# Optimization experiments

Measured on AMD Instinct MI355X. Metric: run time of the kernel, lower is better.

Reference implementation:

```python
import jax, jax.numpy as jnp
import numpy as np

B, N, IN, H, DK, DV, OUT = 8, 1024, 512, 8, 64, 64, 512
SCALE = 1.0 / (DK ** 0.5)


def setup_inputs() -> dict:
    key = jax.random.key(0)
    ks = jax.random.split(key, 10)
    s = lambda fan_in: 1.0 / np.sqrt(fan_in)
    return {
        "x": jax.random.normal(ks[0], (B, N, IN), dtype=jnp.float32),
        "Wv": jax.random.uniform(ks[1], (IN, H * DV), jnp.float32, -s(IN), s(IN)),
        "bv": jax.random.uniform(ks[2], (H * DV,), jnp.float32, -s(IN), s(IN)),
        "Wk": jax.random.uniform(ks[3], (IN, H * DK), jnp.float32, -s(IN), s(IN)),
        "bk": jax.random.uniform(ks[4], (H * DK,), jnp.float32, -s(IN), s(IN)),
        "Wq": jax.random.uniform(ks[5], (IN, H * DK), jnp.float32, -s(IN), s(IN)),
        "bq": jax.random.uniform(ks[6], (H * DK,), jnp.float32, -s(IN), s(IN)),
        "Wo": jax.random.uniform(ks[7], (H * DV, OUT), jnp.float32, -s(H * DV), s(H * DV)),
        "bo": jax.random.uniform(ks[8], (OUT,), jnp.float32, -s(H * DV), s(H * DV)),
        "mask": jax.random.randint(ks[9], (B, N, N), 0, 2, dtype=jnp.int32),
    }


def reference(x, Wv, bv, Wk, bk, Wq, bq, Wo, bo, mask):
    # projections -> (B, N, H, d), vkq activation = relu
    v = jax.nn.relu((x @ Wv + bv).reshape(B, N, H, DV))
    q = jax.nn.relu((x @ Wq + bq).reshape(B, N, H, DK))
    k = jax.nn.relu((x @ Wk + bk).reshape(B, N, H, DK))
    # (B, H, N, d)
    q, k, v = (t.transpose(0, 2, 1, 3) for t in (q, k, v))
    # raw attention weights (returned pre-mask, pre-softmax): (B, H, N, N)
    att_weights = jnp.einsum("bhqd,bhkd->bhqk", q, k) * SCALE
    att = jnp.where(mask[:, None, :, :] == 0, -1e9, att_weights)
    att = jax.nn.softmax(att, axis=-1)
    out = jnp.einsum("bhqk,bhkd->bhqd", att, v) + v  # residual add of v
    out = out.transpose(0, 2, 1, 3).reshape(B, N, H * DV)
    out = jax.nn.relu(out @ Wo + bo)  # final activation = relu
    return out, att_weights
```

## Files before the change

kernel.cpp:

```cpp
#include <hip/hip_runtime.h>
#include <hip/hip_bf16.h>

typedef __attribute__((ext_vector_type(8))) short short8;
typedef __attribute__((ext_vector_type(4))) float f32x4;

#define DEV static __device__ __forceinline__

DEV unsigned short f2bf(float f) {
  union { float f; unsigned u; } v; v.f = f;
  unsigned r = v.u + 0x7FFFu + ((v.u >> 16) & 1u);
  return (unsigned short)(r >> 16);
}
DEV float bf2f(unsigned short b) {
  union { unsigned u; float f; } v; v.u = ((unsigned)b) << 16;
  return v.f;
}

DEV unsigned cvtpk_bf16(float lo, float hi) {
  unsigned r;
  asm("v_cvt_pk_bf16_f32 %0, %1, %2" : "=v"(r) : "v"(lo), "v"(hi));
  return r;
}

DEV void gld_lds16(const void* g, void* l) {
  __builtin_amdgcn_global_load_lds(
      (const __attribute__((address_space(1))) unsigned int*)g,
      (__attribute__((address_space(3))) unsigned int*)l, 16, 0, 0);
}

DEV short8 lds_read8(const unsigned short* base, int byteoff) {
  return *reinterpret_cast<const short8*>(reinterpret_cast<const char*>(base) + byteoff);
}

__global__ __launch_bounds__(256) void cast_x_kernel(const float* __restrict__ x,
                                                     unsigned short* __restrict__ xb, int n4) {
  int i = blockIdx.x * blockDim.x + threadIdx.x;
  if (i >= n4) return;
  float4 v = reinterpret_cast<const float4*>(x)[i];
  ushort4 o;
  o.x = f2bf(v.x); o.y = f2bf(v.y); o.z = f2bf(v.z); o.w = f2bf(v.w);
  reinterpret_cast<ushort4*>(xb)[i] = o;
}

__global__ __launch_bounds__(256) void mask_prep_kernel(const int* __restrict__ mask,
                                                        unsigned char* __restrict__ mb) {
  int i = blockIdx.x * 256 + threadIdx.x;
  int4 m4 = reinterpret_cast<const int4*>(mask)[i];
  unsigned v = (m4.x ? 1u : 0u) | ((m4.y ? 1u : 0u) << 8) |
               ((m4.z ? 1u : 0u) << 16) | ((m4.w ? 1u : 0u) << 24);
  reinterpret_cast<unsigned*>(mb)[i] = v;
}

__global__ __launch_bounds__(256) void transpose_w_kernel(
    const float* __restrict__ W0, const float* __restrict__ W1,
    const float* __restrict__ W2, const float* __restrict__ W3,
    unsigned short* __restrict__ T0, unsigned short* __restrict__ T1,
    unsigned short* __restrict__ T2, unsigned short* __restrict__ T3) {
  const float* W = blockIdx.z == 0 ? W0 : blockIdx.z == 1 ? W1 : blockIdx.z == 2 ? W2 : W3;
  unsigned short* T = blockIdx.z == 0 ? T0 : blockIdx.z == 1 ? T1 : blockIdx.z == 2 ? T2 : T3;
  __shared__ unsigned short tile[32][33];
  int tx = threadIdx.x & 31, ty = threadIdx.x >> 5;
  int n0 = blockIdx.x * 32, k0 = blockIdx.y * 32;
#pragma unroll
  for (int i = 0; i < 32; i += 8)
    tile[ty + i][tx] = f2bf(W[(size_t)(k0 + ty + i) * 512 + n0 + tx]);
  __syncthreads();
#pragma unroll
  for (int i = 0; i < 32; i += 8)
    T[(size_t)(n0 + ty + i) * 512 + k0 + tx] = tile[tx][ty + i];
}

__global__ __launch_bounds__(256) void gemm_proj_kernel(
    const unsigned short* __restrict__ xb,
    const unsigned short* __restrict__ WqT, const unsigned short* __restrict__ WkT,
    const unsigned short* __restrict__ WvT,
    const float* __restrict__ bq, const float* __restrict__ bk, const float* __restrict__ bv,
    unsigned short* __restrict__ qn, unsigned short* __restrict__ kn,
    unsigned short* __restrict__ vn, unsigned short* __restrict__ vT) {
  const int z = blockIdx.z;
  const unsigned short* Wt = z == 0 ? WqT : z == 1 ? WkT : WvT;
  const float* bias = z == 0 ? bq : z == 1 ? bk : bv;
  unsigned short* outp = z == 0 ? qn : z == 1 ? kn : vn;

  __shared__ unsigned short smem[17408];
  unsigned short* As = smem;
  unsigned short* Bs = smem + 4096;

  const int tid = threadIdx.x;
  const int lane = tid & 63;
  const int w = tid >> 6;
  const int wm = w >> 1, wn = w & 1;
  const int lr = lane & 15;
  const int g = lane >> 4;

  const int m0 = blockIdx.x * 128;
  const int n0 = blockIdx.y * 128;

  f32x4 acc[4][4];
#pragma unroll
  for (int i = 0; i < 4; ++i)
#pragma unroll
    for (int j = 0; j < 4; ++j) acc[i][j] = (f32x4){0.f, 0.f, 0.f, 0.f};

  for (int kt = 0; kt < 16; ++kt) {
    const int k0 = kt * 32;
    __syncthreads();
#pragma unroll
    for (int p = 0; p < 2; ++p) {
      int slot = tid + 256 * p;
      int r = slot >> 2;
      int kg = (slot & 3) ^ ((r >> 1) & 3);
      unsigned short* ldsA = As + (size_t)((tid >> 6) + 4 * p) * 512;
      unsigned short* ldsB = Bs + (size_t)((tid >> 6) + 4 * p) * 512;
      gld_lds16(xb + (size_t)(m0 + r) * 512 + k0 + kg * 8, ldsA);
      gld_lds16(Wt + (size_t)(n0 + r) * 512 + k0 + kg * 8, ldsB);
    }
    __syncthreads();
    short8 af[4], bfr[4];
#pragma unroll
    for (int mi = 0; mi < 4; ++mi) {
      int r = wm * 64 + mi * 16 + lr;
      af[mi] = lds_read8(As, (r * 64 + g * 16) ^ (((r >> 1) & 3) << 4));
    }
#pragma unroll
    for (int ni = 0; ni < 4; ++ni) {
      int r = wn * 64 + ni * 16 + lr;
      bfr[ni] = lds_read8(Bs, (r * 64 + g * 16) ^ (((r >> 1) & 3) << 4));
    }
#pragma unroll
    for (int mi = 0; mi < 4; ++mi)
#pragma unroll
      for (int ni = 0; ni < 4; ++ni)
        acc[mi][ni] = __builtin_amdgcn_mfma_f32_16x16x32_bf16(af[mi], bfr[ni], acc[mi][ni], 0, 0, 0);
  }
  __syncthreads();

  float biasv[4];
#pragma unroll
  for (int ni = 0; ni < 4; ++ni) biasv[ni] = bias[n0 + wn * 64 + ni * 16 + lr];

#pragma unroll
  for (int mi = 0; mi < 4; ++mi) {
    int rowb = m0 + wm * 64 + mi * 16 + g * 4;
#pragma unroll
    for (int ni = 0; ni < 4; ++ni) {
      int c = n0 + wn * 64 + ni * 16 + lr;
      int h = c >> 6, d = c & 63;
#pragma unroll
      for (int rr = 0; rr < 4; ++rr) {
        float vf = acc[mi][ni][rr] + biasv[ni];
        vf = vf > 0.f ? vf : 0.f;
        unsigned short bvv = f2bf(vf);
        int row = rowb + rr;
        int b = row >> 10, tok = row & 1023;
        outp[((size_t)(b * 8 + h) * 1024 + tok) * 64 + d] = bvv;
        if (z == 2) {
          int cl = wn * 64 + ni * 16 + lr;
          int rl = wm * 64 + mi * 16 + g * 4 + rr;
          smem[cl * 136 + rl] = bvv;
        }
      }
    }
  }
  if (z == 2) {
    __syncthreads();
    int cl = tid >> 1, half = tid & 1;
    int gc = n0 + cl, h = gc >> 6, d = gc & 63;
    int b = m0 >> 10;
    int tokbase = (m0 & 1023) + half * 64;
    size_t base = (size_t)(b * 8 + h) * 65536 + (size_t)d * 1024 + tokbase;
    const unsigned short* src = smem + cl * 136 + half * 64;
#pragma unroll
    for (int j = 0; j < 8; ++j) {
      short8 v8 = *reinterpret_cast<const short8*>(src + j * 8);
      *reinterpret_cast<short8*>(vT + base + j * 8) = v8;
    }
  }
}

__global__ __launch_bounds__(256) void attn_kernel(
    const unsigned short* __restrict__ qg, const unsigned short* __restrict__ kgp,
    const unsigned short* __restrict__ vg, const unsigned short* __restrict__ vTg,
    const unsigned char* __restrict__ mb, float* __restrict__ attw,
    unsigned short* __restrict__ Og) {
  __shared__ unsigned short Ks[2][4096];
  __shared__ unsigned short Vs[2][4096];
  __shared__ unsigned short Ps[4096];

  const int tid = threadIdx.x, lane = tid & 63, w = tid >> 6;
  const int lr = lane & 15, g = lane >> 4;

  const int bid = blockIdx.x;
  const int b = bid & 7;
  const int idx = bid >> 3;
  const int h = idx >> 4;
  const int qc = idx & 15;
  const int bh = b * 8 + h;

  const int qw = qc * 64 + w * 16;
  const size_t qbase = (size_t)bh * 65536;
  const int gq = qw + lr;

  const unsigned short* kbase = kgp + qbase;
  const unsigned short* vbase = vTg + qbase;

  const int srow0 = w * 8 + (lane >> 3);
  const int sseg = lane & 7;

  short8 aq[2];
#pragma unroll
  for (int dc = 0; dc < 2; ++dc)
    aq[dc] = *reinterpret_cast<const short8*>(qg + qbase + (size_t)gq * 64 + dc * 32 + g * 8);

  f32x4 o[4];
#pragma unroll
  for (int di = 0; di < 4; ++di) o[di] = (f32x4){0.f, 0.f, 0.f, 0.f};
  float lsum = 0.f;

  unsigned short* Pw = Ps + w * 1024;
  const unsigned char* mp = mb + ((size_t)(b * 1024 + gq)) * 1024 + g * 4;
  float* awp = attw + ((size_t)bh * 1024 + gq) * 1024 + g * 4;

#pragma unroll
  for (int p = 0; p < 2; ++p) {
    int rr = srow0 + 32 * p;
    int sk = sseg ^ (rr & 7);
    gld_lds16(kbase + (size_t)rr * 64 + sk * 8, reinterpret_cast<char*>(Ks[0]) + (w + 4 * p) * 1024);
    gld_lds16(vbase + (size_t)rr * 1024 + sk * 8, reinterpret_cast<char*>(Vs[0]) + (w + 4 * p) * 1024);
  }
  asm volatile("s_waitcnt vmcnt(0)" ::: "memory");
  __builtin_amdgcn_sched_barrier(0);
  __builtin_amdgcn_s_barrier();

  int cur = 0;
  for (int t = 0; t < 16; ++t) {
    const int kv0 = t * 64;

    unsigned mk[4];
#pragma unroll
    for (int ni = 0; ni < 4; ++ni)
      mk[ni] = *reinterpret_cast<const unsigned*>(mp + kv0 + ni * 16);
    __builtin_amdgcn_sched_barrier(0);

    if (t < 15) {
      const int kn0 = kv0 + 64;
      unsigned short* Kn = Ks[cur ^ 1];
      unsigned short* Vn = Vs[cur ^ 1];
#pragma unroll
      for (int p = 0; p < 2; ++p) {
        int rr = srow0 + 32 * p;
        int sk = sseg ^ (rr & 7);
        gld_lds16(kbase + (size_t)(kn0 + rr) * 64 + sk * 8,
                  reinterpret_cast<char*>(Kn) + (w + 4 * p) * 1024);
        gld_lds16(vbase + (size_t)rr * 1024 + kn0 + sk * 8,
                  reinterpret_cast<char*>(Vn) + (w + 4 * p) * 1024);
      }
    }
    __builtin_amdgcn_sched_barrier(0);

    const unsigned short* Kc = Ks[cur];
    const unsigned short* Vc = Vs[cur];

    f32x4 s[4];
    __builtin_amdgcn_s_setprio(1);
#pragma unroll
    for (int ni = 0; ni < 4; ++ni) {
      int row = ni * 16 + lr;
      s[ni] = (f32x4){0.f, 0.f, 0.f, 0.f};
#pragma unroll
      for (int dc = 0; dc < 2; ++dc) {
        short8 ak = lds_read8(Kc, (row * 128 + dc * 64 + g * 16) ^ ((row & 7) << 4));
        s[ni] = __builtin_amdgcn_mfma_f32_16x16x32_bf16(ak, aq[dc], s[ni], 0, 0, 0);
      }
    }
    __builtin_amdgcn_s_setprio(0);

#pragma unroll
    for (int ni = 0; ni < 4; ++ni) {
      f32x4 sv = s[ni] * 0.125f;
      *reinterpret_cast<f32x4*>(awp + kv0 + ni * 16) = sv;
      unsigned m = mk[ni];
      float p0 = (m & 0x000000FFu) ? __expf(sv[0] - 16.f) : 0.f;
      float p1 = (m & 0x0000FF00u) ? __expf(sv[1] - 16.f) : 0.f;
      float p2 = (m & 0x00FF0000u) ? __expf(sv[2] - 16.f) : 0.f;
      float p3 = (m & 0xFF000000u) ? __expf(sv[3] - 16.f) : 0.f;
      lsum += (p0 + p1) + (p2 + p3);
      uint2 pk = make_uint2(cvtpk_bf16(p0, p1), cvtpk_bf16(p2, p3));
      int pbyte = (lr * 128 + ni * 32 + g * 8) ^ ((lr & 7) << 4);
      *reinterpret_cast<uint2*>(reinterpret_cast<char*>(Pw) + pbyte) = pk;
    }

    __builtin_amdgcn_s_setprio(1);
#pragma unroll
    for (int kc = 0; kc < 2; ++kc) {
      short8 ap = lds_read8(Pw, (lr * 128 + kc * 64 + g * 16) ^ ((lr & 7) << 4));
#pragma unroll
      for (int di = 0; di < 4; ++di) {
        int rd = di * 16 + lr;
        short8 bv8 = lds_read8(Vc, (rd * 128 + kc * 64 + g * 16) ^ ((rd & 7) << 4));
        o[di] = __builtin_amdgcn_mfma_f32_16x16x32_bf16(ap, bv8, o[di], 0, 0, 0);
      }
    }
    __builtin_amdgcn_s_setprio(0);

    asm volatile("s_waitcnt vmcnt(4)" ::: "memory");
    __builtin_amdgcn_sched_barrier(0);
    __builtin_amdgcn_s_barrier();
    __builtin_amdgcn_sched_barrier(0);
    cur ^= 1;
  }

  float l = lsum;
  l += __shfl_xor(l, 16);
  l += __shfl_xor(l, 32);

#pragma unroll
  for (int rr = 0; rr < 4; ++rr) {
    int gq2 = qw + g * 4 + rr;
    float lq = __shfl(l, g * 4 + rr);
    float inv = 1.f / lq;
#pragma unroll
    for (int di = 0; di < 4; ++di) {
      int gd = di * 16 + lr;
      float ov = o[di][rr] * inv + bf2f(vg[qbase + (size_t)gq2 * 64 + gd]);
      Og[((size_t)(b * 1024 + gq2)) * 512 + h * 64 + gd] = f2bf(ov);
    }
  }
}

__global__ __launch_bounds__(256) void gemm_out_kernel(
    const unsigned short* __restrict__ Ab, const unsigned short* __restrict__ WoT,
    const float* __restrict__ bo, float* __restrict__ outp) {
  __shared__ unsigned short smem[8192];
  unsigned short* As = smem;
  unsigned short* Bs = smem + 4096;

  const int tid = threadIdx.x;
  const int lane = tid & 63;
  const int w = tid >> 6;
  const int wm = w >> 1, wn = w & 1;
  const int lr = lane & 15;
  const int g = lane >> 4;
  const int m0 = blockIdx.x * 128;
  const int n0 = blockIdx.y * 128;

  f32x4 acc[4][4];
#pragma unroll
  for (int i = 0; i < 4; ++i)
#pragma unroll
    for (int j = 0; j < 4; ++j) acc[i][j] = (f32x4){0.f, 0.f, 0.f, 0.f};

  for (int kt = 0; kt < 16; ++kt) {
    const int k0 = kt * 32;
    __syncthreads();
#pragma unroll
    for (int p = 0; p < 2; ++p) {
      int slot = tid + 256 * p;
      int r = slot >> 2;
      int kg = (slot & 3) ^ ((r >> 1) & 3);
      unsigned short* ldsA = As + (size_t)((tid >> 6) + 4 * p) * 512;
      unsigned short* ldsB = Bs + (size_t)((tid >> 6) + 4 * p) * 512;
      gld_lds16(Ab + (size_t)(m0 + r) * 512 + k0 + kg * 8, ldsA);
      gld_lds16(WoT + (size_t)(n0 + r) * 512 + k0 + kg * 8, ldsB);
    }
    __syncthreads();
    short8 af[4], bfr[4];
#pragma unroll
    for (int mi = 0; mi < 4; ++mi) {
      int r = wm * 64 + mi * 16 + lr;
      af[mi] = lds_read8(As, (r * 64 + g * 16) ^ (((r >> 1) & 3) << 4));
    }
#pragma unroll
    for (int ni = 0; ni < 4; ++ni) {
      int r = wn * 64 + ni * 16 + lr;
      bfr[ni] = lds_read8(Bs, (r * 64 + g * 16) ^ (((r >> 1) & 3) << 4));
    }
#pragma unroll
    for (int mi = 0; mi < 4; ++mi)
#pragma unroll
      for (int ni = 0; ni < 4; ++ni)
        acc[mi][ni] = __builtin_amdgcn_mfma_f32_16x16x32_bf16(af[mi], bfr[ni], acc[mi][ni], 0, 0, 0);
  }

  float biasv[4];
#pragma unroll
  for (int ni = 0; ni < 4; ++ni) biasv[ni] = bo[n0 + wn * 64 + ni * 16 + lr];
#pragma unroll
  for (int mi = 0; mi < 4; ++mi) {
    int rowb = m0 + wm * 64 + mi * 16 + g * 4;
#pragma unroll
    for (int ni = 0; ni < 4; ++ni) {
      int c = n0 + wn * 64 + ni * 16 + lr;
#pragma unroll
      for (int rr = 0; rr < 4; ++rr) {
        float vf = acc[mi][ni][rr] + biasv[ni];
        outp[(size_t)(rowb + rr) * 512 + c] = vf > 0.f ? vf : 0.f;
      }
    }
  }
}

extern "C" void kernel_launch(void* const* d_in, const int* in_sizes, int n_in,
                              void* d_out, int out_size, void* d_ws, size_t ws_size,
                              hipStream_t stream) {
  const float* x = (const float*)d_in[0];
  const float* Wv = (const float*)d_in[1];
  const float* bv = (const float*)d_in[2];
  const float* Wk = (const float*)d_in[3];
  const float* bk = (const float*)d_in[4];
  const float* Wq = (const float*)d_in[5];
  const float* bq = (const float*)d_in[6];
  const float* Wo = (const float*)d_in[7];
  const float* bo = (const float*)d_in[8];
  const int* mask = (const int*)d_in[9];

  char* ws = (char*)d_ws;
  unsigned short* xb  = (unsigned short*)(ws);
  unsigned char*  mbb = (unsigned char*)(ws);
  unsigned short* WqT = (unsigned short*)(ws + 8388608);
  unsigned short* WkT = (unsigned short*)(ws + 8912896);
  unsigned short* WvT = (unsigned short*)(ws + 9437184);
  unsigned short* WoT = (unsigned short*)(ws + 9961472);
  unsigned short* qn  = (unsigned short*)(ws + 10485760);
  unsigned short* kn  = (unsigned short*)(ws + 18874368);
  unsigned short* vn  = (unsigned short*)(ws + 27262976);
  unsigned short* vT  = (unsigned short*)(ws + 35651584);
  unsigned short* Og  = (unsigned short*)(ws + 44040192);

  float* outp = (float*)d_out;
  float* attw = (float*)d_out + 4194304;

  cast_x_kernel<<<4096, 256, 0, stream>>>(x, xb, 1048576);

  dim3 tg(16, 16, 4);
  transpose_w_kernel<<<tg, 256, 0, stream>>>(Wq, Wk, Wv, Wo, WqT, WkT, WvT, WoT);

  dim3 gp(64, 4, 3);
  gemm_proj_kernel<<<gp, 256, 0, stream>>>(xb, WqT, WkT, WvT, bq, bk, bv, qn, kn, vn, vT);

  mask_prep_kernel<<<8192, 256, 0, stream>>>(mask, mbb);

  attn_kernel<<<1024, 256, 0, stream>>>(qn, kn, vn, vT, mbb, attw, Og);

  dim3 go(64, 4);
  gemm_out_kernel<<<go, 256, 0, stream>>>(Og, WoT, bo, outp);
}
```

Measured before the change: 145.0 us.

## Process two query subtiles per wave to reuse K/V tiles, halve attention grid

```diff
diff --git a/kernel.cpp b/kernel.cpp
--- a/kernel.cpp
+++ b/kernel.cpp
@@ -185,7 +185,7 @@
     unsigned short* __restrict__ Og) {
   __shared__ unsigned short Ks[2][4096];
   __shared__ unsigned short Vs[2][4096];
-  __shared__ unsigned short Ps[4096];
+  __shared__ unsigned short Ps[8192];
 
   const int tid = threadIdx.x, lane = tid & 63, w = tid >> 6;
   const int lr = lane & 15, g = lane >> 4;
@@ -193,13 +193,12 @@
   const int bid = blockIdx.x;
   const int b = bid & 7;
   const int idx = bid >> 3;
-  const int h = idx >> 4;
-  const int qc = idx & 15;
+  const int h = idx >> 3;
+  const int qc = idx & 7;
   const int bh = b * 8 + h;
 
-  const int qw = qc * 64 + w * 16;
+  const int qw = qc * 128 + w * 32;
   const size_t qbase = (size_t)bh * 65536;
-  const int gq = qw + lr;
 
   const unsigned short* kbase = kgp + qbase;
   const unsigned short* vbase = vTg + qbase;
@@ -207,19 +206,26 @@
   const int srow0 = w * 8 + (lane >> 3);
   const int sseg = lane & 7;
 
-  short8 aq[2];
-#pragma unroll
-  for (int dc = 0; dc < 2; ++dc)
-    aq[dc] = *reinterpret_cast<const short8*>(qg + qbase + (size_t)gq * 64 + dc * 32 + g * 8);
-
-  f32x4 o[4];
-#pragma unroll
-  for (int di = 0; di < 4; ++di) o[di] = (f32x4){0.f, 0.f, 0.f, 0.f};
-  float lsum = 0.f;
-
-  unsigned short* Pw = Ps + w * 1024;
-  const unsigned char* mp = mb + ((size_t)(b * 1024 + gq)) * 1024 + g * 4;
-  float* awp = attw + ((size_t)bh * 1024 + gq) * 1024 + g * 4;
+  short8 aq[2][2];
+#pragma unroll
+  for (int mi = 0; mi < 2; ++mi)
+#pragma unroll
+    for (int dc = 0; dc < 2; ++dc)
+      aq[mi][dc] = *reinterpret_cast<const short8*>(
+          qg + qbase + (size_t)(qw + mi * 16 + lr) * 64 + dc * 32 + g * 8);
+
+  f32x4 o[2][4];
+#pragma unroll
+  for (int mi = 0; mi < 2; ++mi)
+#pragma unroll
+    for (int di = 0; di < 4; ++di) o[mi][di] = (f32x4){0.f, 0.f, 0.f, 0.f};
+  float lsum[2] = {0.f, 0.f};
+
+  unsigned short* Pw = Ps + w * 2048;
+  const unsigned char* mp0 = mb + ((size_t)(b * 1024 + qw + lr)) * 1024 + g * 4;
+  const unsigned char* mp1 = mp0 + 16 * 1024;
+  float* awp0 = attw + ((size_t)bh * 1024 + qw + lr) * 1024 + g * 4;
+  float* awp1 = awp0 + 16 * 1024;
 
 #pragma unroll
   for (int p = 0; p < 2; ++p) {
@@ -236,10 +242,13 @@
   for (int t = 0; t < 16; ++t) {
     const int kv0 = t * 64;
 
-    unsigned mk[4];
-#pragma unroll
-    for (int ni = 0; ni < 4; ++ni)
-      mk[ni] = *reinterpret_cast<const unsigned*>(mp + kv0 + ni * 16);
+    unsigned mk[2][4];
+#pragma unroll
+    for (int mi = 0; mi < 2; ++mi)
+#pragma unroll
+      for (int ni = 0; ni < 4; ++ni)
+        mk[mi][ni] = __builtin_nontemporal_load(reinterpret_cast<const unsigned*>(
+            (mi ? mp1 : mp0) + kv0 + ni * 16));
     __builtin_amdgcn_sched_barrier(0);
 
     if (t < 15) {
@@ -261,69 +270,78 @@
     const unsigned short* Kc = Ks[cur];
     const unsigned short* Vc = Vs[cur];
 
-    f32x4 s[4];
+    f32x4 s[2][4];
     __builtin_amdgcn_s_setprio(1);
 #pragma unroll
     for (int ni = 0; ni < 4; ++ni) {
       int row = ni * 16 + lr;
-      s[ni] = (f32x4){0.f, 0.f, 0.f, 0.f};
+      s[0][ni] = (f32x4){0.f, 0.f, 0.f, 0.f};
+      s[1][ni] = (f32x4){0.f, 0.f, 0.f, 0.f};
 #pragma unroll
       for (int dc = 0; dc < 2; ++dc) {
         short8 ak = lds_read8(Kc, (row * 128 + dc * 64 + g * 16) ^ ((row & 7) << 4));
-        s[ni] = __builtin_amdgcn_mfma_f32_16x16x32_bf16(ak, aq[dc], s[ni], 0, 0, 0);
+        s[0][ni] = __builtin_amdgcn_mfma_f32_16x16x32_bf16(ak, aq[0][dc], s[0][ni], 0, 0, 0);
+        s[1][ni] = __builtin_amdgcn_mfma_f32_16x16x32_bf16(ak, aq[1][dc], s[1][ni], 0, 0, 0);
       }
     }
     __builtin_amdgcn_s_setprio(0);
 
 #pragma unroll
-    for (int ni = 0; ni < 4; ++ni) {
-      f32x4 sv = s[ni] * 0.125f;
-      *reinterpret_cast<f32x4*>(awp + kv0 + ni * 16) = sv;
-      unsigned m = mk[ni];
-      float p0 = (m & 0x000000FFu) ? __expf(sv[0] - 16.f) : 0.f;
-      float p1 = (m & 0x0000FF00u) ? __expf(sv[1] - 16.f) : 0.f;
-      float p2 = (m & 0x00FF0000u) ? __expf(sv[2] - 16.f) : 0.f;
-      float p3 = (m & 0xFF000000u) ? __expf(sv[3] - 16.f) : 0.f;
-      lsum += (p0 + p1) + (p2 + p3);
-      uint2 pk = make_uint2(cvtpk_bf16(p0, p1), cvtpk_bf16(p2, p3));
-      int pbyte = (lr * 128 + ni * 32 + g * 8) ^ ((lr & 7) << 4);
-      *reinterpret_cast<uint2*>(reinterpret_cast<char*>(Pw) + pbyte) = pk;
-    }
+    for (int mi = 0; mi < 2; ++mi)
+#pragma unroll
+      for (int ni = 0; ni < 4; ++ni) {
+        f32x4 sv = s[mi][ni] * 0.125f;
+        __builtin_nontemporal_store(
+            sv, reinterpret_cast<f32x4*>((mi ? awp1 : awp0) + kv0 + ni * 16));
+        unsigned m = mk[mi][ni];
+        float p0 = (m & 0x000000FFu) ? __expf(sv[0] - 16.f) : 0.f;
+        float p1 = (m & 0x0000FF00u) ? __expf(sv[1] - 16.f) : 0.f;
+        float p2 = (m & 0x00FF0000u) ? __expf(sv[2] - 16.f) : 0.f;
+        float p3 = (m & 0xFF000000u) ? __expf(sv[3] - 16.f) : 0.f;
+        lsum[mi] += (p0 + p1) + (p2 + p3);
+        uint2 pk = make_uint2(cvtpk_bf16(p0, p1), cvtpk_bf16(p2, p3));
+        int pbyte = (mi * 2048 + lr * 128 + ni * 32 + g * 8) ^ ((lr & 7) << 4);
+        *reinterpret_cast<uint2*>(reinterpret_cast<char*>(Pw) + pbyte) = pk;
+      }
 
     __builtin_amdgcn_s_setprio(1);
 #pragma unroll
     for (int kc = 0; kc < 2; ++kc) {
-      short8 ap = lds_read8(Pw, (lr * 128 + kc * 64 + g * 16) ^ ((lr & 7) << 4));
+      short8 ap0 = lds_read8(Pw, (lr * 128 + kc * 64 + g * 16) ^ ((lr & 7) << 4));
+      short8 ap1 = lds_read8(Pw, (2048 + lr * 128 + kc * 64 + g * 16) ^ ((lr & 7) << 4));
 #pragma unroll
       for (int di = 0; di < 4; ++di) {
         int rd = di * 16 + lr;
         short8 bv8 = lds_read8(Vc, (rd * 128 + kc * 64 + g * 16) ^ ((rd & 7) << 4));
-        o[di] = __builtin_amdgcn_mfma_f32_16x16x32_bf16(ap, bv8, o[di], 0, 0, 0);
+        o[0][di] = __builtin_amdgcn_mfma_f32_16x16x32_bf16(ap0, bv8, o[0][di], 0, 0, 0);
+        o[1][di] = __builtin_amdgcn_mfma_f32_16x16x32_bf16(ap1, bv8, o[1][di], 0, 0, 0);
       }
     }
     __builtin_amdgcn_s_setprio(0);
 
-    asm volatile("s_waitcnt vmcnt(4)" ::: "memory");
+    asm volatile("s_waitcnt vmcnt(8)" ::: "memory");
     __builtin_amdgcn_sched_barrier(0);
     __builtin_amdgcn_s_barrier();
     __builtin_amdgcn_sched_barrier(0);
     cur ^= 1;
   }
 
-  float l = lsum;
-  l += __shfl_xor(l, 16);
-  l += __shfl_xor(l, 32);
-
-#pragma unroll
-  for (int rr = 0; rr < 4; ++rr) {
-    int gq2 = qw + g * 4 + rr;
-    float lq = __shfl(l, g * 4 + rr);
-    float inv = 1.f / lq;
-#pragma unroll
-    for (int di = 0; di < 4; ++di) {
-      int gd = di * 16 + lr;
-      float ov = o[di][rr] * inv + bf2f(vg[qbase + (size_t)gq2 * 64 + gd]);
-      Og[((size_t)(b * 1024 + gq2)) * 512 + h * 64 + gd] = f2bf(ov);
+#pragma unroll
+  for (int mi = 0; mi < 2; ++mi) {
+    float l = lsum[mi];
+    l += __shfl_xor(l, 16);
+    l += __shfl_xor(l, 32);
+#pragma unroll
+    for (int rr = 0; rr < 4; ++rr) {
+      int gq2 = qw + mi * 16 + g * 4 + rr;
+      float lq = __shfl(l, g * 4 + rr);
+      float inv = 1.f / lq;
+#pragma unroll
+      for (int di = 0; di < 4; ++di) {
+        int gd = di * 16 + lr;
+        float ov = o[mi][di][rr] * inv + bf2f(vg[qbase + (size_t)gq2 * 64 + gd]);
+        Og[((size_t)(b * 1024 + gq2)) * 512 + h * 64 + gd] = f2bf(ov);
+      }
     }
   }
 }
@@ -440,7 +458,7 @@
 
   mask_prep_kernel<<<8192, 256, 0, stream>>>(mask, mbb);
 
-  attn_kernel<<<1024, 256, 0, stream>>>(qn, kn, vn, vT, mbb, attw, Og);
+  attn_kernel<<<512, 256, 0, stream>>>(qn, kn, vn, vT, mbb, attw, Og);
 
   dim3 go(64, 4);
   gemm_out_kernel<<<go, 256, 0, stream>>>(Og, WoT, bo, outp);
```

New measurement: 233.3 us. +60.9%, slower.

## Fuse prep kernels into one launch and use 512-thread attention blocks

Applied to the files above, without the earlier changes.

```diff
diff --git a/kernel.cpp b/kernel.cpp
--- a/kernel.cpp
+++ b/kernel.cpp
@@ -32,14 +32,43 @@
   return *reinterpret_cast<const short8*>(reinterpret_cast<const char*>(base) + byteoff);
 }
 
-__global__ __launch_bounds__(256) void cast_x_kernel(const float* __restrict__ x,
-                                                     unsigned short* __restrict__ xb, int n4) {
-  int i = blockIdx.x * blockDim.x + threadIdx.x;
-  if (i >= n4) return;
-  float4 v = reinterpret_cast<const float4*>(x)[i];
-  ushort4 o;
-  o.x = f2bf(v.x); o.y = f2bf(v.y); o.z = f2bf(v.z); o.w = f2bf(v.w);
-  reinterpret_cast<ushort4*>(xb)[i] = o;
+__global__ __launch_bounds__(256) void prep_kernel(
+    const float* __restrict__ x, unsigned short* __restrict__ xb,
+    const float* __restrict__ W0, const float* __restrict__ W1,
+    const float* __restrict__ W2, const float* __restrict__ W3,
+    unsigned short* __restrict__ T0, unsigned short* __restrict__ T1,
+    unsigned short* __restrict__ T2, unsigned short* __restrict__ T3,
+    const int* __restrict__ mask, unsigned char* __restrict__ mb) {
+  __shared__ unsigned short tile[32][33];
+  const int bid = blockIdx.x, tid = threadIdx.x;
+  if (bid < 4096) {
+    int i = bid * 256 + tid;
+    float4 v = reinterpret_cast<const float4*>(x)[i];
+    ushort4 o;
+    o.x = f2bf(v.x); o.y = f2bf(v.y); o.z = f2bf(v.z); o.w = f2bf(v.w);
+    reinterpret_cast<ushort4*>(xb)[i] = o;
+  } else if (bid < 5120) {
+    int r = bid - 4096;
+    int z = r >> 8;
+    r &= 255;
+    const float* W = z == 0 ? W0 : z == 1 ? W1 : z == 2 ? W2 : W3;
+    unsigned short* T = z == 0 ? T0 : z == 1 ? T1 : z == 2 ? T2 : T3;
+    int tx = tid & 31, ty = tid >> 5;
+    int n0 = (r & 15) * 32, k0 = (r >> 4) * 32;
+#pragma unroll
+    for (int i = 0; i < 32; i += 8)
+      tile[ty + i][tx] = f2bf(W[(size_t)(k0 + ty + i) * 512 + n0 + tx]);
+    __syncthreads();
+#pragma unroll
+    for (int i = 0; i < 32; i += 8)
+      T[(size_t)(n0 + ty + i) * 512 + k0 + tx] = tile[tx][ty + i];
+  } else {
+    int i = (bid - 5120) * 256 + tid;
+    int4 m4 = reinterpret_cast<const int4*>(mask)[i];
+    unsigned v = (m4.x ? 1u : 0u) | ((m4.y ? 1u : 0u) << 8) |
+                 ((m4.z ? 1u : 0u) << 16) | ((m4.w ? 1u : 0u) << 24);
+    reinterpret_cast<unsigned*>(mb)[i] = v;
+  }
 }
 
 __global__ __launch_bounds__(256) void mask_prep_kernel(const int* __restrict__ mask,
@@ -49,25 +78,6 @@
   unsigned v = (m4.x ? 1u : 0u) | ((m4.y ? 1u : 0u) << 8) |
                ((m4.z ? 1u : 0u) << 16) | ((m4.w ? 1u : 0u) << 24);
   reinterpret_cast<unsigned*>(mb)[i] = v;
-}
-
-__global__ __launch_bounds__(256) void transpose_w_kernel(
-    const float* __restrict__ W0, const float* __restrict__ W1,
-    const float* __restrict__ W2, const float* __restrict__ W3,
-    unsigned short* __restrict__ T0, unsigned short* __restrict__ T1,
-    unsigned short* __restrict__ T2, unsigned short* __restrict__ T3) {
-  const float* W = blockIdx.z == 0 ? W0 : blockIdx.z == 1 ? W1 : blockIdx.z == 2 ? W2 : W3;
-  unsigned short* T = blockIdx.z == 0 ? T0 : blockIdx.z == 1 ? T1 : blockIdx.z == 2 ? T2 : T3;
-  __shared__ unsigned short tile[32][33];
-  int tx = threadIdx.x & 31, ty = threadIdx.x >> 5;
-  int n0 = blockIdx.x * 32, k0 = blockIdx.y * 32;
-#pragma unroll
-  for (int i = 0; i < 32; i += 8)
-    tile[ty + i][tx] = f2bf(W[(size_t)(k0 + ty + i) * 512 + n0 + tx]);
-  __syncthreads();
-#pragma unroll
-  for (int i = 0; i < 32; i += 8)
-    T[(size_t)(n0 + ty + i) * 512 + k0 + tx] = tile[tx][ty + i];
 }
 
 __global__ __launch_bounds__(256) void gemm_proj_kernel(
@@ -178,14 +188,14 @@
   }
 }
 
-__global__ __launch_bounds__(256) void attn_kernel(
+__global__ __launch_bounds__(512) void attn_kernel(
     const unsigned short* __restrict__ qg, const unsigned short* __restrict__ kgp,
     const unsigned short* __restrict__ vg, const unsigned short* __restrict__ vTg,
     const unsigned char* __restrict__ mb, float* __restrict__ attw,
     unsigned short* __restrict__ Og) {
   __shared__ unsigned short Ks[2][4096];
   __shared__ unsigned short Vs[2][4096];
-  __shared__ unsigned short Ps[4096];
+  __shared__ unsigned short Ps[8192];
 
   const int tid = threadIdx.x, lane = tid & 63, w = tid >> 6;
   const int lr = lane & 15, g = lane >> 4;
@@ -193,24 +203,24 @@
   const int bid = blockIdx.x;
   const int b = bid & 7;
   const int idx = bid >> 3;
-  const int h = idx >> 4;
-  const int qc = idx & 15;
+  const int h = idx >> 3;
+  const int qc = idx & 7;
   const int bh = b * 8 + h;
 
-  const int qw = qc * 64 + w * 16;
+  const int qw = qc * 128 + w * 16;
   const size_t qbase = (size_t)bh * 65536;
-  const int gq = qw + lr;
 
   const unsigned short* kbase = kgp + qbase;
   const unsigned short* vbase = vTg + qbase;
 
-  const int srow0 = w * 8 + (lane >> 3);
-  const int sseg = lane & 7;
+  const int srow = w * 8 + (lane >> 3);
+  const int ssw = ((lane & 7) ^ (srow & 7)) * 8;
 
   short8 aq[2];
 #pragma unroll
   for (int dc = 0; dc < 2; ++dc)
-    aq[dc] = *reinterpret_cast<const short8*>(qg + qbase + (size_t)gq * 64 + dc * 32 + g * 8);
+    aq[dc] = *reinterpret_cast<const short8*>(
+        qg + qbase + (size_t)(qw + lr) * 64 + dc * 32 + g * 8);
 
   f32x4 o[4];
 #pragma unroll
@@ -218,16 +228,11 @@
   float lsum = 0.f;
 
   unsigned short* Pw = Ps + w * 1024;
-  const unsigned char* mp = mb + ((size_t)(b * 1024 + gq)) * 1024 + g * 4;
-  float* awp = attw + ((size_t)bh * 1024 + gq) * 1024 + g * 4;
-
-#pragma unroll
-  for (int p = 0; p < 2; ++p) {
-    int rr = srow0 + 32 * p;
-    int sk = sseg ^ (rr & 7);
-    gld_lds16(kbase + (size_t)rr * 64 + sk * 8, reinterpret_cast<char*>(Ks[0]) + (w + 4 * p) * 1024);
-    gld_lds16(vbase + (size_t)rr * 1024 + sk * 8, reinterpret_cast<char*>(Vs[0]) + (w + 4 * p) * 1024);
-  }
+  const unsigned char* mp = mb + ((size_t)(b * 1024 + qw + lr)) * 1024 + g * 4;
+  float* awp = attw + ((size_t)bh * 1024 + qw + lr) * 1024 + g * 4;
+
+  gld_lds16(kbase + (size_t)srow * 64 + ssw, reinterpret_cast<char*>(Ks[0]) + w * 1024);
+  gld_lds16(vbase + (size_t)srow * 1024 + ssw, reinterpret_cast<char*>(Vs[0]) + w * 1024);
   asm volatile("s_waitcnt vmcnt(0)" ::: "memory");
   __builtin_amdgcn_sched_barrier(0);
   __builtin_amdgcn_s_barrier();
@@ -244,17 +249,10 @@
 
     if (t < 15) {
       const int kn0 = kv0 + 64;
-      unsigned short* Kn = Ks[cur ^ 1];
-      unsigned short* Vn = Vs[cur ^ 1];
-#pragma unroll
-      for (int p = 0; p < 2; ++p) {
-        int rr = srow0 + 32 * p;
-        int sk = sseg ^ (rr & 7);
-        gld_lds16(kbase + (size_t)(kn0 + rr) * 64 + sk * 8,
-                  reinterpret_cast<char*>(Kn) + (w + 4 * p) * 1024);
-        gld_lds16(vbase + (size_t)rr * 1024 + kn0 + sk * 8,
-                  reinterpret_cast<char*>(Vn) + (w + 4 * p) * 1024);
-      }
+      gld_lds16(kbase + (size_t)(kn0 + srow) * 64 + ssw,
+                reinterpret_cast<char*>(Ks[cur ^ 1]) + w * 1024);
+      gld_lds16(vbase + (size_t)srow * 1024 + kn0 + ssw,
+                reinterpret_cast<char*>(Vs[cur ^ 1]) + w * 1024);
     }
     __builtin_amdgcn_sched_barrier(0);
 
@@ -416,7 +414,6 @@
 
   char* ws = (char*)d_ws;
   unsigned short* xb  = (unsigned short*)(ws);
-  unsigned char*  mbb = (unsigned char*)(ws);
   unsigned short* WqT = (unsigned short*)(ws + 8388608);
   unsigned short* WkT = (unsigned short*)(ws + 8912896);
   unsigned short* WvT = (unsigned short*)(ws + 9437184);
@@ -427,20 +424,22 @@
   unsigned short* vT  = (unsigned short*)(ws + 35651584);
   unsigned short* Og  = (unsigned short*)(ws + 44040192);
 
+  const size_t MBB_HI = 52428800;
+  const bool big = ws_size >= MBB_HI + 8388608;
+  unsigned char* mbb = big ? (unsigned char*)(ws + MBB_HI) : (unsigned char*)ws;
+
   float* outp = (float*)d_out;
   float* attw = (float*)d_out + 4194304;
 
-  cast_x_kernel<<<4096, 256, 0, stream>>>(x, xb, 1048576);
-
-  dim3 tg(16, 16, 4);
-  transpose_w_kernel<<<tg, 256, 0, stream>>>(Wq, Wk, Wv, Wo, WqT, WkT, WvT, WoT);
+  prep_kernel<<<big ? 13312 : 5120, 256, 0, stream>>>(
+      x, xb, Wq, Wk, Wv, Wo, WqT, WkT, WvT, WoT, mask, mbb);
 
   dim3 gp(64, 4, 3);
   gemm_proj_kernel<<<gp, 256, 0, stream>>>(xb, WqT, WkT, WvT, bq, bk, bv, qn, kn, vn, vT);
 
-  mask_prep_kernel<<<8192, 256, 0, stream>>>(mask, mbb);
-
-  attn_kernel<<<1024, 256, 0, stream>>>(qn, kn, vn, vT, mbb, attw, Og);
+  if (!big) mask_prep_kernel<<<8192, 256, 0, stream>>>(mask, mbb);
+
+  attn_kernel<<<512, 512, 0, stream>>>(qn, kn, vn, vT, mbb, attw, Og);
 
   dim3 go(64, 4);
   gemm_out_kernel<<<go, 256, 0, stream>>>(Og, WoT, bo, outp);
```

After: 132.6 us. 8.5% less time.
